# Optimization experiments

Hardware: AMD Instinct MI355X
Metric: run time of the kernel (lower is better)

The kernel has to match this reference:

```python
import jax, jax.numpy as jnp
import numpy as np

B, L, H, E, K = 64, 200, 256, 8, 2
LN_EPS = 1e-5

def setup_inputs() -> dict:
    key = jax.random.key(0)
    ks = jax.random.split(key, 24)
    r = lambda k, *s: jax.random.normal(k, s, dtype=jnp.float32)
    w = lambda k, *s: 0.02 * jax.random.normal(k, s, dtype=jnp.float32)
    return {
        'text_emb': r(ks[0], B, L, H),
        'img_emb': r(ks[1], B, L, H),
        'item_emb': r(ks[2], B, L, H),
        'noise_t': r(ks[3], B, L, H),
        'noise_i': r(ks[4], B, L, H),
        'W_mu_t': w(ks[5], H, H), 'b_mu_t': jnp.zeros((H,), jnp.float32),
        'W_sg_t': w(ks[6], H, H), 'b_sg_t': jnp.zeros((H,), jnp.float32),
        'W_mu_i': w(ks[7], H, H), 'b_mu_i': jnp.zeros((H,), jnp.float32),
        'W_sg_i': w(ks[8], H, H), 'b_sg_i': jnp.zeros((H,), jnp.float32),
        'W_gate': w(ks[9], H, E), 'b_gate': jnp.zeros((E,), jnp.float32),
        'W_texp': w(ks[10], E, H, H), 'b_texp': jnp.zeros((E, H), jnp.float32),
        'W_iexp': w(ks[11], E, H, H), 'b_iexp': jnp.zeros((E, H), jnp.float32),
        'W_fuse': w(ks[12], 2 * H, H), 'b_fuse': jnp.zeros((H,), jnp.float32),
        'ln_g': jnp.ones((H,), jnp.float32), 'ln_b': jnp.zeros((H,), jnp.float32),
    }

def _topk_routing(z, W_gate, b_gate):
    # softmax over experts, keep top-k, renormalize (matches torch scatter_ version)
    weights = jax.nn.softmax(z @ W_gate + b_gate, axis=-1)   # [B,L,E]
    top_w, idx = jax.lax.top_k(weights, K)                   # [B,L,K]
    sparse = jnp.sum(jax.nn.one_hot(idx, E, dtype=weights.dtype) * top_w[..., None], axis=-2)
    return sparse / (jnp.sum(sparse, axis=-1, keepdims=True) + 1e-8)

def _layernorm(x, g, b):
    mu = jnp.mean(x, axis=-1, keepdims=True)
    var = jnp.mean(jnp.square(x - mu), axis=-1, keepdims=True)
    return (x - mu) * jax.lax.rsqrt(var + LN_EPS) * g + b

def reference(text_emb, img_emb, item_emb, noise_t, noise_i,
              W_mu_t, b_mu_t, W_sg_t, b_sg_t, W_mu_i, b_mu_i, W_sg_i, b_sg_i,
              W_gate, b_gate, W_texp, b_texp, W_iexp, b_iexp,
              W_fuse, b_fuse, ln_g, ln_b):
    # VAE-style reparameterization per modality
    t_mu = text_emb @ W_mu_t + b_mu_t
    t_sigma = jnp.exp(text_emb @ W_sg_t + b_sg_t)
    i_mu = img_emb @ W_mu_i + b_mu_i
    i_sigma = jnp.exp(img_emb @ W_sg_i + b_sg_i)
    t_z = t_mu + t_sigma * noise_t
    i_z = i_mu + i_sigma * noise_i
    # top-k gating
    t_gate = _topk_routing(t_z, W_gate, b_gate)   # [B,L,E]
    i_gate = _topk_routing(i_z, W_gate, b_gate)
    # dense all-expert stack + gated combine
    t_experts = jnp.einsum('blh,ehd->bled', t_z, W_texp) + b_texp  # [B,L,E,H]
    t_out = jnp.einsum('bled,ble->bld', t_experts, t_gate)
    i_experts = jnp.einsum('blh,ehd->bled', i_z, W_iexp) + b_iexp
    i_out = jnp.einsum('bled,ble->bld', i_experts, i_gate)
    # fusion: Linear(2H->H) -> LayerNorm -> ReLU, residual with item_emb
    cat = jnp.concatenate([t_out, i_out], axis=-1)
    fused = jax.nn.relu(_layernorm(cat @ W_fuse + b_fuse, ln_g, ln_b))
    fusion = item_emb + fused
    return fusion, t_mu, t_sigma, i_mu, i_sigma
```

## Files before the change

kernel.cpp:

```cpp
#include <hip/hip_runtime.h>
#include <hip/hip_bf16.h>
#include <math.h>

#define NTOK 12800
#define HD 256
#define SOUT (NTOK * HD)

typedef __attribute__((ext_vector_type(8))) short short8_t;
typedef __attribute__((ext_vector_type(4))) float f32x4;

__device__ __forceinline__ unsigned short f2b(float f) {
    union { float f; unsigned u; } v; v.f = f;
    unsigned r = (v.u + 0x7FFFu + ((v.u >> 16) & 1u)) >> 16;
    return (unsigned short)r;
}
__device__ __forceinline__ float b2f(unsigned short s) {
    union { unsigned u; float f; } v; v.u = ((unsigned)s) << 16;
    return v.f;
}

__global__ __launch_bounds__(256) void prepW_kernel(
    const float* __restrict__ W_texp, const float* __restrict__ W_iexp,
    const float* __restrict__ W_mu_t, const float* __restrict__ W_sg_t,
    const float* __restrict__ W_mu_i, const float* __restrict__ W_sg_i,
    const float* __restrict__ W_fuse,
    unsigned short* __restrict__ wt_t, unsigned short* __restrict__ wt_i,
    unsigned short* __restrict__ wt_f,
    unsigned short* __restrict__ wpk_th, unsigned short* __restrict__ wpk_tl,
    unsigned short* __restrict__ wpk_ih, unsigned short* __restrict__ wpk_il)
{
    const int z = blockIdx.y;
    const float* src;
    unsigned short* dsth;
    unsigned short* dstl = nullptr;
    int dstride = 256, koff = 0, rowoff = 0;
    if (z < 8)       { src = W_texp + (size_t)z * 65536;       dsth = wt_t + (size_t)z * 65536; }
    else if (z < 16) { src = W_iexp + (size_t)(z - 8) * 65536; dsth = wt_i + (size_t)(z - 8) * 65536; }
    else if (z == 16){ src = W_mu_t; dsth = wpk_th; dstl = wpk_tl; }
    else if (z == 17){ src = W_sg_t; dsth = wpk_th; dstl = wpk_tl; rowoff = 256; }
    else if (z == 18){ src = W_mu_i; dsth = wpk_ih; dstl = wpk_il; }
    else if (z == 19){ src = W_sg_i; dsth = wpk_ih; dstl = wpk_il; rowoff = 256; }
    else if (z == 20){ src = W_fuse;         dsth = wt_f; dstride = 512; koff = 0;   }
    else             { src = W_fuse + 65536; dsth = wt_f; dstride = 512; koff = 256; }

    const int tk = (blockIdx.x >> 2) * 64;
    const int td = (blockIdx.x & 3) * 64;
    __shared__ float T[64][68];
    const int t = threadIdx.x;
    {
        const int r = t >> 2, c0 = (t & 3) * 16;
        const float* s = &src[(size_t)(tk + r) * 256 + td + c0];
#pragma unroll
        for (int j = 0; j < 4; ++j)
            *reinterpret_cast<float4*>(&T[r][c0 + j * 4]) =
                *reinterpret_cast<const float4*>(&s[j * 4]);
    }
    __syncthreads();
    {
        const int d = t & 63, kc = (t >> 6) * 16;
        union { unsigned short s[16]; short8_t v[2]; } uh, ul;
#pragma unroll
        for (int j = 0; j < 16; ++j) {
            const float x = T[kc + j][d];
            uh.s[j] = f2b(x);
            ul.s[j] = f2b(x - b2f(uh.s[j]));
        }
        unsigned short* p = &dsth[(size_t)(rowoff + td + d) * dstride + koff + tk + kc];
        *reinterpret_cast<short8_t*>(p) = uh.v[0];
        *reinterpret_cast<short8_t*>(p + 8) = uh.v[1];
        if (dstl) {
            unsigned short* q = &dstl[(size_t)(rowoff + td + d) * 256 + tk + kc];
            *reinterpret_cast<short8_t*>(q) = ul.v[0];
            *reinterpret_cast<short8_t*>(q + 8) = ul.v[1];
        }
    }
}

__global__ __launch_bounds__(256) void cvt_kernel(
    const float* __restrict__ text, const float* __restrict__ img,
    unsigned short* __restrict__ ah_t, unsigned short* __restrict__ al_t,
    unsigned short* __restrict__ ah_i, unsigned short* __restrict__ al_i)
{
    const int mod = blockIdx.y;
    const float* src = mod ? img : text;
    unsigned short* dh = mod ? ah_i : ah_t;
    unsigned short* dl = mod ? al_i : al_t;
    const size_t base = ((size_t)blockIdx.x * 256 + threadIdx.x) * 8;
    const float4 v0 = *reinterpret_cast<const float4*>(&src[base]);
    const float4 v1 = *reinterpret_cast<const float4*>(&src[base + 4]);
    const float x[8] = { v0.x, v0.y, v0.z, v0.w, v1.x, v1.y, v1.z, v1.w };
    union { unsigned short u[8]; short8_t v; } qh, ql;
#pragma unroll
    for (int c = 0; c < 8; ++c) {
        qh.u[c] = f2b(x[c]);
        ql.u[c] = f2b(x[c] - b2f(qh.u[c]));
    }
    *reinterpret_cast<short8_t*>(&dh[base]) = qh.v;
    *reinterpret_cast<short8_t*>(&dl[base]) = ql.v;
}

__global__ __launch_bounds__(256) void reparam_mfma_kernel(
    const unsigned short* __restrict__ ah_t, const unsigned short* __restrict__ al_t,
    const unsigned short* __restrict__ ah_i, const unsigned short* __restrict__ al_i,
    const unsigned short* __restrict__ wpk_th, const unsigned short* __restrict__ wpk_tl,
    const unsigned short* __restrict__ wpk_ih, const unsigned short* __restrict__ wpk_il,
    const float* __restrict__ b_mu_t, const float* __restrict__ b_sg_t,
    const float* __restrict__ b_mu_i, const float* __restrict__ b_sg_i,
    float* __restrict__ o_tmu, float* __restrict__ o_tsig,
    float* __restrict__ o_imu, float* __restrict__ o_isig)
{
    const int mod = blockIdx.z;
    const unsigned short* Ah = mod ? ah_i : ah_t;
    const unsigned short* Al = mod ? al_i : al_t;
    const unsigned short* Wh = mod ? wpk_ih : wpk_th;
    const unsigned short* Wl = mod ? wpk_il : wpk_tl;
    const float* bmu = mod ? b_mu_i : b_mu_t;
    const float* bsg = mod ? b_sg_i : b_sg_t;
    float* omu = mod ? o_imu : o_tmu;
    float* osg = mod ? o_isig : o_tsig;

    __shared__ __align__(16) unsigned short AhS[2][4][64][8];
    __shared__ __align__(16) unsigned short AlS[2][4][64][8];
    __shared__ __align__(16) unsigned short BhS[2][4][128][8];
    __shared__ __align__(16) unsigned short BlS[2][4][128][8];

    const int tid = threadIdx.x;
    const int lane = tid & 63;
    const int w = tid >> 6;
    const int wr = w >> 1, wc = w & 1;
    const int lg = lane >> 4;
    const int lr = lane & 15;
    const int m0 = blockIdx.x * 64;
    const int n0 = blockIdx.y * 128;

    const int ar = tid >> 2, akc = tid & 3;
    const int bn = tid >> 1, bk0 = (tid & 1) * 2;

    {
        *reinterpret_cast<short8_t*>(&AhS[0][akc][ar][0]) =
            *reinterpret_cast<const short8_t*>(&Ah[(size_t)(m0 + ar) * HD + akc * 8]);
        *reinterpret_cast<short8_t*>(&AlS[0][akc][ar][0]) =
            *reinterpret_cast<const short8_t*>(&Al[(size_t)(m0 + ar) * HD + akc * 8]);
#pragma unroll
        for (int j = 0; j < 2; ++j) {
            const int kc = bk0 + j;
            *reinterpret_cast<short8_t*>(&BhS[0][kc][bn][0]) =
                *reinterpret_cast<const short8_t*>(&Wh[(size_t)(n0 + bn) * HD + kc * 8]);
            *reinterpret_cast<short8_t*>(&BlS[0][kc][bn][0]) =
                *reinterpret_cast<const short8_t*>(&Wl[(size_t)(n0 + bn) * HD + kc * 8]);
        }
    }
    __syncthreads();

    f32x4 acc[2][4];
#pragma unroll
    for (int mi = 0; mi < 2; ++mi)
#pragma unroll
        for (int ni = 0; ni < 4; ++ni)
            acc[mi][ni] = (f32x4){0.f, 0.f, 0.f, 0.f};

    for (int ks = 0; ks < 8; ++ks) {
        const int cur = ks & 1;
        short8_t rah, ral, rbh[2], rbl[2];
        if (ks < 7) {
            const int k1 = (ks + 1) * 32;
            rah = *reinterpret_cast<const short8_t*>(&Ah[(size_t)(m0 + ar) * HD + k1 + akc * 8]);
            ral = *reinterpret_cast<const short8_t*>(&Al[(size_t)(m0 + ar) * HD + k1 + akc * 8]);
#pragma unroll
            for (int j = 0; j < 2; ++j) {
                const int kc = bk0 + j;
                rbh[j] = *reinterpret_cast<const short8_t*>(&Wh[(size_t)(n0 + bn) * HD + k1 + kc * 8]);
                rbl[j] = *reinterpret_cast<const short8_t*>(&Wl[(size_t)(n0 + bn) * HD + k1 + kc * 8]);
            }
        }
        short8_t ahf[2], alf[2], bhf[4], blf[4];
#pragma unroll
        for (int mi = 0; mi < 2; ++mi) {
            ahf[mi] = *reinterpret_cast<const short8_t*>(&AhS[cur][lg][wr * 32 + mi * 16 + lr][0]);
            alf[mi] = *reinterpret_cast<const short8_t*>(&AlS[cur][lg][wr * 32 + mi * 16 + lr][0]);
        }
#pragma unroll
        for (int ni = 0; ni < 4; ++ni) {
            bhf[ni] = *reinterpret_cast<const short8_t*>(&BhS[cur][lg][wc * 64 + ni * 16 + lr][0]);
            blf[ni] = *reinterpret_cast<const short8_t*>(&BlS[cur][lg][wc * 64 + ni * 16 + lr][0]);
        }
#pragma unroll
        for (int mi = 0; mi < 2; ++mi)
#pragma unroll
            for (int ni = 0; ni < 4; ++ni) {
                acc[mi][ni] = __builtin_amdgcn_mfma_f32_16x16x32_bf16(ahf[mi], bhf[ni], acc[mi][ni], 0, 0, 0);
                acc[mi][ni] = __builtin_amdgcn_mfma_f32_16x16x32_bf16(ahf[mi], blf[ni], acc[mi][ni], 0, 0, 0);
                acc[mi][ni] = __builtin_amdgcn_mfma_f32_16x16x32_bf16(alf[mi], bhf[ni], acc[mi][ni], 0, 0, 0);
            }
        if (ks < 7) {
            const int nxt = cur ^ 1;
            *reinterpret_cast<short8_t*>(&AhS[nxt][akc][ar][0]) = rah;
            *reinterpret_cast<short8_t*>(&AlS[nxt][akc][ar][0]) = ral;
#pragma unroll
            for (int j = 0; j < 2; ++j) {
                const int kc = bk0 + j;
                *reinterpret_cast<short8_t*>(&BhS[nxt][kc][bn][0]) = rbh[j];
                *reinterpret_cast<short8_t*>(&BlS[nxt][kc][bn][0]) = rbl[j];
            }
        }
        __syncthreads();
    }

    const bool is_sg = (n0 >= 256);
    float bv[4];
    int cc[4];
#pragma unroll
    for (int ni = 0; ni < 4; ++ni) {
        const int dpk = n0 + wc * 64 + ni * 16 + lr;
        cc[ni] = is_sg ? dpk - 256 : dpk;
        bv[ni] = is_sg ? bsg[cc[ni]] : bmu[cc[ni]];
    }
    float* outp = is_sg ? osg : omu;
#pragma unroll
    for (int mi = 0; mi < 2; ++mi)
#pragma unroll
        for (int r = 0; r < 4; ++r) {
            const int row = m0 + wr * 32 + mi * 16 + lg * 4 + r;
#pragma unroll
            for (int ni = 0; ni < 4; ++ni) {
                const float v = acc[mi][ni][r] + bv[ni];
                outp[(size_t)row * HD + cc[ni]] = is_sg ? expf(v) : v;
            }
        }
}

__global__ __launch_bounds__(256) void gate_kernel(
    const float* __restrict__ o_tmu, const float* __restrict__ o_tsig,
    const float* __restrict__ o_imu, const float* __restrict__ o_isig,
    const float* __restrict__ noise_t, const float* __restrict__ noise_i,
    const float* __restrict__ Wg, const float* __restrict__ bg,
    float* __restrict__ t_gate, float* __restrict__ i_gate,
    unsigned short* __restrict__ tzb, unsigned short* __restrict__ izb)
{
    const int mod = blockIdx.y;
    const float* mu    = mod ? o_imu  : o_tmu;
    const float* sig   = mod ? o_isig : o_tsig;
    const float* noise = mod ? noise_i : noise_t;
    float* gate        = mod ? i_gate : t_gate;
    unsigned short* zb = mod ? izb : tzb;

    const int lane = threadIdx.x & 63;
    const int n = blockIdx.x * 4 + (threadIdx.x >> 6);
    const size_t off = (size_t)n * HD + lane * 4;
    const float4 m4 = *reinterpret_cast<const float4*>(&mu[off]);
    const float4 s4 = *reinterpret_cast<const float4*>(&sig[off]);
    const float4 n4 = *reinterpret_cast<const float4*>(&noise[off]);
    const float zz[4] = { fmaf(s4.x, n4.x, m4.x), fmaf(s4.y, n4.y, m4.y),
                          fmaf(s4.z, n4.z, m4.z), fmaf(s4.w, n4.w, m4.w) };
    ushort4 zb4;
    zb4.x = f2b(zz[0]); zb4.y = f2b(zz[1]); zb4.z = f2b(zz[2]); zb4.w = f2b(zz[3]);
    *reinterpret_cast<ushort4*>(&zb[off]) = zb4;

    float lg[8];
#pragma unroll
    for (int e = 0; e < 8; ++e) lg[e] = 0.f;
#pragma unroll
    for (int i = 0; i < 4; ++i) {
        const float* wr = &Wg[(size_t)(lane * 4 + i) * 8];
        const float4 w0 = *reinterpret_cast<const float4*>(wr);
        const float4 w1 = *reinterpret_cast<const float4*>(wr + 4);
        lg[0] = fmaf(zz[i], w0.x, lg[0]); lg[1] = fmaf(zz[i], w0.y, lg[1]);
        lg[2] = fmaf(zz[i], w0.z, lg[2]); lg[3] = fmaf(zz[i], w0.w, lg[3]);
        lg[4] = fmaf(zz[i], w1.x, lg[4]); lg[5] = fmaf(zz[i], w1.y, lg[5]);
        lg[6] = fmaf(zz[i], w1.z, lg[6]); lg[7] = fmaf(zz[i], w1.w, lg[7]);
    }
#pragma unroll
    for (int off2 = 32; off2; off2 >>= 1)
#pragma unroll
        for (int e = 0; e < 8; ++e) lg[e] += __shfl_down(lg[e], off2);

    if (lane == 0) {
        float m = -1e30f;
#pragma unroll
        for (int e = 0; e < 8; ++e) { lg[e] += bg[e]; m = fmaxf(m, lg[e]); }
        float p[8], s = 0.f;
#pragma unroll
        for (int e = 0; e < 8; ++e) { p[e] = expf(lg[e] - m); s += p[e]; }
        const float inv_s = 1.f / s;
#pragma unroll
        for (int e = 0; e < 8; ++e) p[e] *= inv_s;
        int e1 = 0;
#pragma unroll
        for (int e = 1; e < 8; ++e) if (p[e] > p[e1]) e1 = e;
        int e2 = (e1 == 0) ? 1 : 0;
#pragma unroll
        for (int e = 0; e < 8; ++e) if (e != e1 && p[e] > p[e2]) e2 = e;
        const float denom = 1.f / (p[e1] + p[e2] + 1e-8f);
        float g[8];
#pragma unroll
        for (int e = 0; e < 8; ++e) g[e] = 0.f;
        g[e1] = p[e1] * denom; g[e2] = p[e2] * denom;
        float* gr = &gate[(size_t)n * 8];
        *reinterpret_cast<float4*>(gr)     = make_float4(g[0], g[1], g[2], g[3]);
        *reinterpret_cast<float4*>(gr + 4) = make_float4(g[4], g[5], g[6], g[7]);
    }
}

__global__ __launch_bounds__(256) void expert_mfma_kernel(
    const unsigned short* __restrict__ tzb, const unsigned short* __restrict__ izb,
    const unsigned short* __restrict__ wt_t, const unsigned short* __restrict__ wt_i,
    const float* __restrict__ bx_t, const float* __restrict__ bx_i,
    const float* __restrict__ g_t, const float* __restrict__ g_i,
    unsigned short* __restrict__ out_t, unsigned short* __restrict__ out_i)
{
    const int mod = blockIdx.z;
    const unsigned short* Zb = mod ? izb : tzb;
    const unsigned short* Wt = mod ? wt_i : wt_t;
    const float* bx   = mod ? bx_i : bx_t;
    const float* gate = mod ? g_i  : g_t;
    unsigned short* outp = mod ? out_i : out_t;

    __shared__ __align__(16) unsigned short AlS[32][64][8];
    __shared__ __align__(16) unsigned short BlS[2][4][128][8];
    __shared__ float gld[64][8];

    const int tid = threadIdx.x;
    const int lane = tid & 63;
    const int w = tid >> 6;
    const int wr = w >> 1, wc = w & 1;
    const int lg = lane >> 4;
    const int lr = lane & 15;
    const int m0 = blockIdx.x * 64;
    const int n0 = blockIdx.y * 128;

    const int bn = tid >> 1, bk0 = (tid & 1) * 2;

    {
        const int r = tid >> 2, kcg = tid & 3;
        const unsigned short* src = &Zb[(size_t)(m0 + r) * HD + kcg * 64];
#pragma unroll
        for (int j = 0; j < 8; ++j)
            *reinterpret_cast<short8_t*>(&AlS[kcg * 8 + j][r][0]) =
                *reinterpret_cast<const short8_t*>(&src[j * 8]);
    }
    if (tid < 128)
        reinterpret_cast<float4*>(&gld[0][0])[tid] =
            reinterpret_cast<const float4*>(&gate[(size_t)m0 * 8])[tid];
    {
        const unsigned short* We = Wt + (size_t)n0 * HD;
#pragma unroll
        for (int j = 0; j < 2; ++j) {
            const int kc = bk0 + j;
            *reinterpret_cast<short8_t*>(&BlS[0][kc][bn][0]) =
                *reinterpret_cast<const short8_t*>(&We[(size_t)bn * HD + kc * 8]);
        }
    }
    __syncthreads();

    f32x4 acc[2][4], accT[2][4];
#pragma unroll
    for (int mi = 0; mi < 2; ++mi)
#pragma unroll
        for (int ni = 0; ni < 4; ++ni) {
            acc[mi][ni]  = (f32x4){0.f, 0.f, 0.f, 0.f};
            accT[mi][ni] = (f32x4){0.f, 0.f, 0.f, 0.f};
        }

    for (int kk = 0; kk < 64; ++kk) {
        const int cur = kk & 1;
        const int e = kk >> 3, ks = kk & 7;
        short8_t rb[2];
        if (kk < 63) {
            const int e2 = (kk + 1) >> 3, ks2 = (kk + 1) & 7;
            const unsigned short* We2 = Wt + (size_t)e2 * HD * HD + (size_t)n0 * HD;
#pragma unroll
            for (int j = 0; j < 2; ++j) {
                const int kc = bk0 + j;
                rb[j] = *reinterpret_cast<const short8_t*>(
                    &We2[(size_t)bn * HD + ks2 * 32 + kc * 8]);
            }
        }
        short8_t af[2], bf[4];
#pragma unroll
        for (int mi = 0; mi < 2; ++mi)
            af[mi] = *reinterpret_cast<const short8_t*>(
                &AlS[ks * 4 + lg][wr * 32 + mi * 16 + lr][0]);
#pragma unroll
        for (int ni = 0; ni < 4; ++ni)
            bf[ni] = *reinterpret_cast<const short8_t*>(
                &BlS[cur][lg][wc * 64 + ni * 16 + lr][0]);
#pragma unroll
        for (int mi = 0; mi < 2; ++mi)
#pragma unroll
            for (int ni = 0; ni < 4; ++ni)
                acc[mi][ni] = __builtin_amdgcn_mfma_f32_16x16x32_bf16(
                    af[mi], bf[ni], acc[mi][ni], 0, 0, 0);
        if (kk < 63) {
            const int nxt = cur ^ 1;
#pragma unroll
            for (int j = 0; j < 2; ++j)
                *reinterpret_cast<short8_t*>(&BlS[nxt][bk0 + j][bn][0]) = rb[j];
        }
        if (ks == 7) {
#pragma unroll
            for (int mi = 0; mi < 2; ++mi) {
                const int rb2 = wr * 32 + mi * 16 + lg * 4;
                const float gv0 = gld[rb2 + 0][e];
                const float gv1 = gld[rb2 + 1][e];
                const float gv2 = gld[rb2 + 2][e];
                const float gv3 = gld[rb2 + 3][e];
#pragma unroll
                for (int ni = 0; ni < 4; ++ni) {
                    const float bv = bx[(size_t)e * HD + n0 + wc * 64 + ni * 16 + lr];
                    accT[mi][ni][0] += gv0 * (acc[mi][ni][0] + bv);
                    accT[mi][ni][1] += gv1 * (acc[mi][ni][1] + bv);
                    accT[mi][ni][2] += gv2 * (acc[mi][ni][2] + bv);
                    accT[mi][ni][3] += gv3 * (acc[mi][ni][3] + bv);
                    acc[mi][ni] = (f32x4){0.f, 0.f, 0.f, 0.f};
                }
            }
        }
        __syncthreads();
    }

#pragma unroll
    for (int mi = 0; mi < 2; ++mi)
#pragma unroll
        for (int ni = 0; ni < 4; ++ni)
#pragma unroll
            for (int r = 0; r < 4; ++r)
                outp[(size_t)(m0 + wr * 32 + mi * 16 + lg * 4 + r) * HD
                     + n0 + wc * 64 + ni * 16 + lr] = f2b(accT[mi][ni][r]);
}

__global__ __launch_bounds__(256) void fusegemm_mfma_kernel(
    const unsigned short* __restrict__ t_outb, const unsigned short* __restrict__ i_outb,
    const unsigned short* __restrict__ wtf, const float* __restrict__ bfuse,
    float* __restrict__ fused)
{
    __shared__ __align__(16) unsigned short AS[2][8][64][8];
    __shared__ __align__(16) unsigned short BS[2][8][128][8];

    const int tid = threadIdx.x;
    const int lane = tid & 63;
    const int w = tid >> 6;
    const int wr = w >> 1, wc = w & 1;
    const int lg = lane >> 4;
    const int lr = lane & 15;
    const int m0 = blockIdx.x * 64;
    const int n0 = blockIdx.y * 128;

    const int ar = tid >> 2, akc0 = (tid & 3) * 2;
    const int bn = tid >> 1, bkc0 = (tid & 1) * 4;

    {
        const unsigned short* base = t_outb;
#pragma unroll
        for (int j = 0; j < 2; ++j) {
            const int kc = akc0 + j;
            *reinterpret_cast<short8_t*>(&AS[0][kc][ar][0]) =
                *reinterpret_cast<const short8_t*>(&base[(size_t)(m0 + ar) * HD + kc * 8]);
        }
#pragma unroll
        for (int j = 0; j < 4; ++j) {
            const int kc = bkc0 + j;
            *reinterpret_cast<short8_t*>(&BS[0][kc][bn][0]) =
                *reinterpret_cast<const short8_t*>(&wtf[(size_t)(n0 + bn) * 512 + kc * 8]);
        }
    }
    __syncthreads();

    f32x4 acc[2][4];
#pragma unroll
    for (int mi = 0; mi < 2; ++mi)
#pragma unroll
        for (int ni = 0; ni < 4; ++ni)
            acc[mi][ni] = (f32x4){0.f, 0.f, 0.f, 0.f};

    for (int ks = 0; ks < 8; ++ks) {
        const int cur = ks & 1;
        short8_t ra[2], rbv[4];
        if (ks < 7) {
            const int ks2 = ks + 1;
            const unsigned short* base = (ks2 < 4) ? t_outb : i_outb;
            const int kloc = (ks2 & 3) * 64;
#pragma unroll
            for (int j = 0; j < 2; ++j) {
                const int kc = akc0 + j;
                ra[j] = *reinterpret_cast<const short8_t*>(
                    &base[(size_t)(m0 + ar) * HD + kloc + kc * 8]);
            }
#pragma unroll
            for (int j = 0; j < 4; ++j) {
                const int kc = bkc0 + j;
                rbv[j] = *reinterpret_cast<const short8_t*>(
                    &wtf[(size_t)(n0 + bn) * 512 + ks2 * 64 + kc * 8]);
            }
        }
#pragma unroll
        for (int s = 0; s < 2; ++s) {
            short8_t af[2], bf[4];
#pragma unroll
            for (int mi = 0; mi < 2; ++mi)
                af[mi] = *reinterpret_cast<const short8_t*>(
                    &AS[cur][s * 4 + lg][wr * 32 + mi * 16 + lr][0]);
#pragma unroll
            for (int ni = 0; ni < 4; ++ni)
                bf[ni] = *reinterpret_cast<const short8_t*>(
                    &BS[cur][s * 4 + lg][wc * 64 + ni * 16 + lr][0]);
#pragma unroll
            for (int mi = 0; mi < 2; ++mi)
#pragma unroll
                for (int ni = 0; ni < 4; ++ni)
                    acc[mi][ni] = __builtin_amdgcn_mfma_f32_16x16x32_bf16(
                        af[mi], bf[ni], acc[mi][ni], 0, 0, 0);
        }
        if (ks < 7) {
            const int nxt = cur ^ 1;
#pragma unroll
            for (int j = 0; j < 2; ++j)
                *reinterpret_cast<short8_t*>(&AS[nxt][akc0 + j][ar][0]) = ra[j];
#pragma unroll
            for (int j = 0; j < 4; ++j)
                *reinterpret_cast<short8_t*>(&BS[nxt][bkc0 + j][bn][0]) = rbv[j];
        }
        __syncthreads();
    }

    float bv[4];
    int cc[4];
#pragma unroll
    for (int ni = 0; ni < 4; ++ni) {
        cc[ni] = n0 + wc * 64 + ni * 16 + lr;
        bv[ni] = bfuse[cc[ni]];
    }
#pragma unroll
    for (int mi = 0; mi < 2; ++mi)
#pragma unroll
        for (int r = 0; r < 4; ++r) {
            const int row = m0 + wr * 32 + mi * 16 + lg * 4 + r;
#pragma unroll
            for (int ni = 0; ni < 4; ++ni)
                fused[(size_t)row * HD + cc[ni]] = acc[mi][ni][r] + bv[ni];
        }
}

__global__ __launch_bounds__(256) void ln_relu_res_kernel(
    const float* __restrict__ fused, const float* __restrict__ g,
    const float* __restrict__ b, const float* __restrict__ item,
    float* __restrict__ fusion)
{
    const int lane = threadIdx.x & 63;
    const int n = blockIdx.x * 4 + (threadIdx.x >> 6);
    const size_t off = (size_t)n * HD + lane * 4;
    const float4 x = *reinterpret_cast<const float4*>(&fused[off]);
    float s = x.x + x.y + x.z + x.w;
    float ss = x.x * x.x + x.y * x.y + x.z * x.z + x.w * x.w;
#pragma unroll
    for (int o = 32; o; o >>= 1) { s += __shfl_xor(s, o); ss += __shfl_xor(ss, o); }
    const float mean = s * (1.f / 256.f);
    const float var = ss * (1.f / 256.f) - mean * mean;
    const float rstd = rsqrtf(var + 1e-5f);
    const float4 gg = *reinterpret_cast<const float4*>(&g[lane * 4]);
    const float4 bb = *reinterpret_cast<const float4*>(&b[lane * 4]);
    const float4 it = *reinterpret_cast<const float4*>(&item[off]);
    float4 o4;
    o4.x = fmaxf((x.x - mean) * rstd * gg.x + bb.x, 0.f) + it.x;
    o4.y = fmaxf((x.y - mean) * rstd * gg.y + bb.y, 0.f) + it.y;
    o4.z = fmaxf((x.z - mean) * rstd * gg.z + bb.z, 0.f) + it.z;
    o4.w = fmaxf((x.w - mean) * rstd * gg.w + bb.w, 0.f) + it.w;
    *reinterpret_cast<float4*>(&fusion[off]) = o4;
}

extern "C" void kernel_launch(void* const* d_in, const int* in_sizes, int n_in,
                              void* d_out, int out_size, void* d_ws, size_t ws_size,
                              hipStream_t stream)
{
    const float* text    = (const float*)d_in[0];
    const float* img     = (const float*)d_in[1];
    const float* item    = (const float*)d_in[2];
    const float* noise_t = (const float*)d_in[3];
    const float* noise_i = (const float*)d_in[4];
    const float* W_mu_t  = (const float*)d_in[5];
    const float* b_mu_t  = (const float*)d_in[6];
    const float* W_sg_t  = (const float*)d_in[7];
    const float* b_sg_t  = (const float*)d_in[8];
    const float* W_mu_i  = (const float*)d_in[9];
    const float* b_mu_i  = (const float*)d_in[10];
    const float* W_sg_i  = (const float*)d_in[11];
    const float* b_sg_i  = (const float*)d_in[12];
    const float* W_gate  = (const float*)d_in[13];
    const float* b_gate  = (const float*)d_in[14];
    const float* W_texp  = (const float*)d_in[15];
    const float* b_texp  = (const float*)d_in[16];
    const float* W_iexp  = (const float*)d_in[17];
    const float* b_iexp  = (const float*)d_in[18];
    const float* W_fuse  = (const float*)d_in[19];
    const float* b_fuse  = (const float*)d_in[20];
    const float* ln_g    = (const float*)d_in[21];
    const float* ln_b    = (const float*)d_in[22];

    float* out    = (float*)d_out;
    float* fusion = out;
    float* o_tmu  = out + (size_t)SOUT;
    float* o_tsig = out + (size_t)2 * SOUT;
    float* o_imu  = out + (size_t)3 * SOUT;
    float* o_isig = out + (size_t)4 * SOUT;

    unsigned short* bufA = (unsigned short*)d_ws;
    unsigned short* bufB = bufA + (size_t)SOUT;
    unsigned short* bufC = bufB + (size_t)SOUT;
    unsigned short* tzb  = bufC + (size_t)2 * SOUT;
    unsigned short* izb  = tzb + (size_t)SOUT;
    float* t_gate = (float*)(izb + (size_t)SOUT);
    float* i_gate = t_gate + (size_t)NTOK * 8;
    unsigned short* wt_t   = (unsigned short*)(i_gate + (size_t)NTOK * 8);
    unsigned short* wt_i   = wt_t + (size_t)8 * 65536;
    unsigned short* wt_f   = wt_i + (size_t)8 * 65536;
    unsigned short* wpk_th = wt_f + (size_t)131072;
    unsigned short* wpk_tl = wpk_th + (size_t)131072;
    unsigned short* wpk_ih = wpk_tl + (size_t)131072;
    unsigned short* wpk_il = wpk_ih + (size_t)131072;

    unsigned short* ah_t = bufA;
    unsigned short* al_t = bufB;
    unsigned short* ah_i = bufC;
    unsigned short* al_i = bufC + (size_t)SOUT;
    unsigned short* t_outb = bufA;
    unsigned short* i_outb = bufB;
    float* fused = (float*)bufC;

    prepW_kernel<<<dim3(16, 22), 256, 0, stream>>>(
        W_texp, W_iexp, W_mu_t, W_sg_t, W_mu_i, W_sg_i, W_fuse,
        wt_t, wt_i, wt_f, wpk_th, wpk_tl, wpk_ih, wpk_il);

    cvt_kernel<<<dim3(SOUT / 2048, 2), 256, 0, stream>>>(
        text, img, ah_t, al_t, ah_i, al_i);

    reparam_mfma_kernel<<<dim3(NTOK / 64, 4, 2), 256, 0, stream>>>(
        ah_t, al_t, ah_i, al_i, wpk_th, wpk_tl, wpk_ih, wpk_il,
        b_mu_t, b_sg_t, b_mu_i, b_sg_i,
        o_tmu, o_tsig, o_imu, o_isig);

    gate_kernel<<<dim3(NTOK / 4, 2), 256, 0, stream>>>(
        o_tmu, o_tsig, o_imu, o_isig, noise_t, noise_i,
        W_gate, b_gate, t_gate, i_gate, tzb, izb);

    expert_mfma_kernel<<<dim3(NTOK / 64, 2, 2), 256, 0, stream>>>(
        tzb, izb, wt_t, wt_i, b_texp, b_iexp, t_gate, i_gate, t_outb, i_outb);

    fusegemm_mfma_kernel<<<dim3(NTOK / 64, 2), 256, 0, stream>>>(
        t_outb, i_outb, wt_f, b_fuse, fused);

    ln_relu_res_kernel<<<NTOK / 4, 256, 0, stream>>>(fused, ln_g, ln_b, item, fusion);
}
```

Measured before the change: 161.2 us.

## Enlarge expert GEMM M-tile to 128 and stage A/B via global_load_lds

The expert GEMM tile grows from 64 to 128 rows per block, so each wave holds a 4x4 accumulator grid and every loaded weight tile is reused across twice as many tokens. Operand staging changes too. Z is no longer preloaded whole into LDS, and A and B k-slices are now double-buffered with direct global-to-LDS 16-byte loads instead of going through registers. This cuts weight traffic and register staging, but doubles accumulator registers, which may lower occupancy, and halves the grid to 400 blocks.

```diff
diff --git a/kernel.cpp b/kernel.cpp
--- a/kernel.cpp
+++ b/kernel.cpp
@@ -17,6 +17,11 @@
 __device__ __forceinline__ float b2f(unsigned short s) {
     union { unsigned u; float f; } v; v.u = ((unsigned)s) << 16;
     return v.f;
+}
+__device__ __forceinline__ void glds16(const void* g, void* l) {
+    __builtin_amdgcn_global_load_lds(
+        (const __attribute__((address_space(1))) void*)g,
+        (__attribute__((address_space(3))) void*)l, 16, 0, 0);
 }
 
 __global__ __launch_bounds__(256) void prepW_kernel(
@@ -315,9 +320,9 @@
     const float* gate = mod ? g_i  : g_t;
     unsigned short* outp = mod ? out_i : out_t;
 
-    __shared__ __align__(16) unsigned short AlS[32][64][8];
-    __shared__ __align__(16) unsigned short BlS[2][4][128][8];
-    __shared__ float gld[64][8];
+    __shared__ __align__(16) unsigned short Ab[2][512][8];
+    __shared__ __align__(16) unsigned short Bb[2][512][8];
+    __shared__ float gld[128][8];
 
     const int tid = threadIdx.x;
     const int lane = tid & 63;
@@ -325,36 +330,35 @@
     const int wr = w >> 1, wc = w & 1;
     const int lg = lane >> 4;
     const int lr = lane & 15;
-    const int m0 = blockIdx.x * 64;
+    const int m0 = blockIdx.x * 128;
     const int n0 = blockIdx.y * 128;
 
-    const int bn = tid >> 1, bk0 = (tid & 1) * 2;
-
-    {
-        const int r = tid >> 2, kcg = tid & 3;
-        const unsigned short* src = &Zb[(size_t)(m0 + r) * HD + kcg * 64];
-#pragma unroll
-        for (int j = 0; j < 8; ++j)
-            *reinterpret_cast<short8_t*>(&AlS[kcg * 8 + j][r][0]) =
-                *reinterpret_cast<const short8_t*>(&src[j * 8]);
-    }
-    if (tid < 128)
-        reinterpret_cast<float4*>(&gld[0][0])[tid] =
-            reinterpret_cast<const float4*>(&gate[(size_t)m0 * 8])[tid];
-    {
-        const unsigned short* We = Wt + (size_t)n0 * HD;
-#pragma unroll
-        for (int j = 0; j < 2; ++j) {
-            const int kc = bk0 + j;
-            *reinterpret_cast<short8_t*>(&BlS[0][kc][bn][0]) =
-                *reinterpret_cast<const short8_t*>(&We[(size_t)bn * HD + kc * 8]);
-        }
-    }
+    reinterpret_cast<float4*>(&gld[0][0])[tid] =
+        reinterpret_cast<const float4*>(&gate[(size_t)m0 * 8])[tid];
+
+    const int c0 = w * 64 + lane;
+    const int row0 = c0 >> 2,          kc0 = c0 & 3;
+    const int row1 = (c0 + 256) >> 2,  kc1 = (c0 + 256) & 3;
+
+#define STAGE(buf, e_, ks_)                                                    \
+    {                                                                          \
+        const unsigned short* We_ = Wt + (size_t)(e_) * 65536 + (size_t)n0 * HD;\
+        glds16(&Zb[(size_t)(m0 + row0) * HD + (ks_) * 32 + kc0 * 8],           \
+               &Ab[buf][w * 64][0]);                                           \
+        glds16(&Zb[(size_t)(m0 + row1) * HD + (ks_) * 32 + kc1 * 8],           \
+               &Ab[buf][256 + w * 64][0]);                                     \
+        glds16(&We_[(size_t)row0 * HD + (ks_) * 32 + kc0 * 8],                 \
+               &Bb[buf][w * 64][0]);                                           \
+        glds16(&We_[(size_t)row1 * HD + (ks_) * 32 + kc1 * 8],                 \
+               &Bb[buf][256 + w * 64][0]);                                     \
+    }
+
+    STAGE(0, 0, 0);
     __syncthreads();
 
-    f32x4 acc[2][4], accT[2][4];
-#pragma unroll
-    for (int mi = 0; mi < 2; ++mi)
+    f32x4 acc[4][4], accT[4][4];
+#pragma unroll
+    for (int mi = 0; mi < 4; ++mi)
 #pragma unroll
         for (int ni = 0; ni < 4; ++ni) {
             acc[mi][ni]  = (f32x4){0.f, 0.f, 0.f, 0.f};
@@ -364,46 +368,33 @@
     for (int kk = 0; kk < 64; ++kk) {
         const int cur = kk & 1;
         const int e = kk >> 3, ks = kk & 7;
-        short8_t rb[2];
         if (kk < 63) {
             const int e2 = (kk + 1) >> 3, ks2 = (kk + 1) & 7;
-            const unsigned short* We2 = Wt + (size_t)e2 * HD * HD + (size_t)n0 * HD;
-#pragma unroll
-            for (int j = 0; j < 2; ++j) {
-                const int kc = bk0 + j;
-                rb[j] = *reinterpret_cast<const short8_t*>(
-                    &We2[(size_t)bn * HD + ks2 * 32 + kc * 8]);
-            }
-        }
-        short8_t af[2], bf[4];
-#pragma unroll
-        for (int mi = 0; mi < 2; ++mi)
+            STAGE(cur ^ 1, e2, ks2);
+        }
+        short8_t af[4], bf[4];
+#pragma unroll
+        for (int mi = 0; mi < 4; ++mi)
             af[mi] = *reinterpret_cast<const short8_t*>(
-                &AlS[ks * 4 + lg][wr * 32 + mi * 16 + lr][0]);
+                &Ab[cur][(wr * 64 + mi * 16 + lr) * 4 + lg][0]);
 #pragma unroll
         for (int ni = 0; ni < 4; ++ni)
             bf[ni] = *reinterpret_cast<const short8_t*>(
-                &BlS[cur][lg][wc * 64 + ni * 16 + lr][0]);
-#pragma unroll
-        for (int mi = 0; mi < 2; ++mi)
+                &Bb[cur][(wc * 64 + ni * 16 + lr) * 4 + lg][0]);
+#pragma unroll
+        for (int mi = 0; mi < 4; ++mi)
 #pragma unroll
             for (int ni = 0; ni < 4; ++ni)
                 acc[mi][ni] = __builtin_amdgcn_mfma_f32_16x16x32_bf16(
                     af[mi], bf[ni], acc[mi][ni], 0, 0, 0);
-        if (kk < 63) {
-            const int nxt = cur ^ 1;
-#pragma unroll
-            for (int j = 0; j < 2; ++j)
-                *reinterpret_cast<short8_t*>(&BlS[nxt][bk0 + j][bn][0]) = rb[j];
-        }
         if (ks == 7) {
 #pragma unroll
-            for (int mi = 0; mi < 2; ++mi) {
-                const int rb2 = wr * 32 + mi * 16 + lg * 4;
-                const float gv0 = gld[rb2 + 0][e];
-                const float gv1 = gld[rb2 + 1][e];
-                const float gv2 = gld[rb2 + 2][e];
-                const float gv3 = gld[rb2 + 3][e];
+            for (int mi = 0; mi < 4; ++mi) {
+                const int rb = wr * 64 + mi * 16 + lg * 4;
+                const float gv0 = gld[rb + 0][e];
+                const float gv1 = gld[rb + 1][e];
+                const float gv2 = gld[rb + 2][e];
+                const float gv3 = gld[rb + 3][e];
 #pragma unroll
                 for (int ni = 0; ni < 4; ++ni) {
                     const float bv = bx[(size_t)e * HD + n0 + wc * 64 + ni * 16 + lr];
@@ -417,14 +408,15 @@
         }
         __syncthreads();
     }
-
-#pragma unroll
-    for (int mi = 0; mi < 2; ++mi)
+#undef STAGE
+
+#pragma unroll
+    for (int mi = 0; mi < 4; ++mi)
 #pragma unroll
         for (int ni = 0; ni < 4; ++ni)
 #pragma unroll
             for (int r = 0; r < 4; ++r)
-                outp[(size_t)(m0 + wr * 32 + mi * 16 + lg * 4 + r) * HD
+                outp[(size_t)(m0 + wr * 64 + mi * 16 + lg * 4 + r) * HD
                      + n0 + wc * 64 + ni * 16 + lr] = f2b(accT[mi][ni][r]);
 }
 
@@ -641,7 +633,7 @@
         o_tmu, o_tsig, o_imu, o_isig, noise_t, noise_i,
         W_gate, b_gate, t_gate, i_gate, tzb, izb);
 
-    expert_mfma_kernel<<<dim3(NTOK / 64, 2, 2), 256, 0, stream>>>(
+    expert_mfma_kernel<<<dim3(NTOK / 128, 2, 2), 256, 0, stream>>>(
         tzb, izb, wt_t, wt_i, b_texp, b_iexp, t_gate, i_gate, t_outb, i_outb);
 
     fusegemm_mfma_kernel<<<dim3(NTOK / 64, 2), 256, 0, stream>>>(
```

New measurement: 152.7 us. 5.3% less time.
